# Optimization experiments

Hardware: AMD Instinct MI355X
Metric: run time of the kernel (lower is better)

The kernel has to match this reference:

```python
import jax, jax.numpy as jnp
import numpy as np

B, N, D = 8, 2048, 1024
A_STDP, TAU_STDP, W_OFF, T_MAX = 0.9, 0.5, 0.9, 1.0
V_TH, EPS = 1.0, 1e-5


def setup_inputs() -> dict:
    key = jax.random.key(0)
    ks = jax.random.split(key, 6)
    s = 0.02
    inp = {"x": jax.random.normal(ks[0], (B, N, D), dtype=jnp.float32)}
    for i, nm in enumerate(["q", "k", "v"]):
        inp[f"W{nm}"] = jax.random.normal(ks[1 + i], (D, D), dtype=jnp.float32) * s
        inp[f"g{nm}"] = jnp.ones((D,), jnp.float32)
        inp[f"b{nm}"] = jnp.zeros((D,), jnp.float32)
        inp[f"m{nm}"] = jnp.zeros((D,), jnp.float32)
        inp[f"v{nm}"] = jnp.ones((D,), jnp.float32)
    inp["Wo"] = jax.random.normal(ks[4], (D, D), dtype=jnp.float32) * s
    inp["bo"] = jnp.zeros((D,), jnp.float32)
    return inp


def _proj(x, W, g, b, m, v):
    # Linear (no bias) -> BatchNorm1d (inference, running stats) -> LIF first step
    h = x @ W                                     # [B,N,D]
    h = (h - m) * (g * jax.lax.rsqrt(v + EPS)) + b
    # LIF with mem=None: mem = x, spike = sigmoid(4*(mem - v_th))
    return jax.nn.sigmoid(4.0 * (h - V_TH))


def reference(x, Wq, gq, bq, mq, vq, Wk, gk, bk, mk, vk, Wv, gv, bv, mv, vv, Wo, bo):
    Q = _proj(x, Wq, gq, bq, mq, vq)
    K = _proj(x, Wk, gk, bk, mk, vk)
    V = _proj(x, Wv, gv, bv, mv, vv)
    t_Q = T_MAX * (1.0 - Q.mean(axis=-1, keepdims=True))   # [B,N,1]
    t_K = T_MAX * (1.0 - K.mean(axis=-1, keepdims=True))   # [B,N,1]
    delta_t = t_Q - jnp.swapaxes(t_K, 1, 2)                 # [B,N,N]
    f_stdp = A_STDP * jnp.exp(-jnp.abs(delta_t) / TAU_STDP)
    A = jnp.where(delta_t < 0, f_stdp, -f_stdp) + W_OFF     # [B,N,N]
    return (A @ V) @ Wo + bo                                # [B,N,D]
```

## Files before the change

kernel.cpp:

```cpp
#include <hip/hip_runtime.h>

#define B_ 8
#define N_ 2048
#define D_ 1024
#define M_ (B_*N_)
#define SEGS 64
#define EPB (4096/SEGS)
#define CW 256

typedef __attribute__((ext_vector_type(8))) short short8;
typedef __attribute__((ext_vector_type(4))) float floatx4;

__device__ __forceinline__ ushort f2bf(float f) {
  unsigned u = __builtin_bit_cast(unsigned, f);
  return (ushort)((u + 0x7fffu + ((u >> 16) & 1u)) >> 16);
}
__device__ __forceinline__ float bf2f(ushort u) {
  return __builtin_bit_cast(float, ((unsigned)u) << 16);
}
__device__ __forceinline__ void gload16(const void* g, void* l) {
  __builtin_amdgcn_global_load_lds(
      (const __attribute__((address_space(1))) unsigned*)g,
      (__attribute__((address_space(3))) unsigned*)l, 16, 0, 0);
}
__device__ __forceinline__ float sig4(float h) {
  return 1.0f / (1.0f + __expf(4.0f - 4.0f*h));
}

__global__ __launch_bounds__(256) void conv_x_k(const float4* __restrict__ x,
                                                ushort4* __restrict__ o) {
  int i = blockIdx.x * 256 + threadIdx.x;
  float4 f = x[i];
  ushort4 u;
  u.x = f2bf(f.x); u.y = f2bf(f.y); u.z = f2bf(f.z); u.w = f2bf(f.w);
  o[i] = u;
}

__global__ __launch_bounds__(256) void transpose_k(
    const float* __restrict__ Wq, const float* __restrict__ Wk,
    const float* __restrict__ Wv, const float* __restrict__ Wo,
    ushort* __restrict__ W3T, ushort* __restrict__ WoT) {
  __shared__ float tile[32][33];
  int z = blockIdx.z;
  const float* W = (z == 0) ? Wq : (z == 1) ? Wk : (z == 2) ? Wv : Wo;
  ushort* WT = (z < 3) ? (W3T + (size_t)z * D_ * D_) : WoT;
  int tx = threadIdx.x, ty = threadIdx.y;
  int x = blockIdx.x * 32 + tx;
  int y = blockIdx.y * 32 + ty;
#pragma unroll
  for (int j = 0; j < 32; j += 8)
    tile[ty + j][tx] = W[(size_t)(y + j) * D_ + x];
  __syncthreads();
  int x2 = blockIdx.y * 32 + tx;
  int y2 = blockIdx.x * 32 + ty;
#pragma unroll
  for (int j = 0; j < 32; j += 8)
    WT[(size_t)(y2 + j) * D_ + x2] = f2bf(tile[tx][ty + j]);
}

__device__ __forceinline__ void gemm_mainloop(
    const ushort* __restrict__ Ab, const ushort* __restrict__ Bb,
    ushort* As, ushort* Bs, int t, int wm, int wn, int l15, int quad,
    floatx4 acc[4][4])
{
  int srow[4], soff[4];
#pragma unroll
  for (int r = 0; r < 4; r++) {
    int li = r * 256 + t;
    int row = li >> 3, c = li & 7;
    srow[r] = row;
    soff[r] = ((c - row) & 7) * 8;
  }
  for (int k0 = 0; k0 < D_; k0 += 64) {
    __syncthreads();
#pragma unroll
    for (int r = 0; r < 4; r++) {
      int li = r * 256 + t;
      gload16(Ab + (size_t)srow[r] * D_ + k0 + soff[r], (char*)As + li * 16);
      gload16(Bb + (size_t)srow[r] * D_ + k0 + soff[r], (char*)Bs + li * 16);
    }
    __syncthreads();
#pragma unroll
    for (int s = 0; s < 2; s++) {
      short8 af[4], bfr[4];
#pragma unroll
      for (int tm = 0; tm < 4; tm++) {
        int row = wm * 64 + tm * 16 + l15;
        int p = (s * 4 + quad + row) & 7;
        af[tm] = *(const short8*)(As + row * 64 + p * 8);
      }
#pragma unroll
      for (int tn = 0; tn < 4; tn++) {
        int row = wn * 64 + tn * 16 + l15;
        int p = (s * 4 + quad + row) & 7;
        bfr[tn] = *(const short8*)(Bs + row * 64 + p * 8);
      }
#pragma unroll
      for (int tm = 0; tm < 4; tm++)
#pragma unroll
        for (int tn = 0; tn < 4; tn++)
          acc[tm][tn] = __builtin_amdgcn_mfma_f32_16x16x32_bf16(af[tm], bfr[tn], acc[tm][tn], 0, 0, 0);
    }
  }
}

__global__ __launch_bounds__(256) void gemm_qkv_k(
    const ushort* __restrict__ A, const ushort* __restrict__ W3T,
    const float* __restrict__ gq, const float* __restrict__ bq,
    const float* __restrict__ mq, const float* __restrict__ vq,
    const float* __restrict__ gk, const float* __restrict__ bk,
    const float* __restrict__ mk, const float* __restrict__ vk,
    const float* __restrict__ gv, const float* __restrict__ bv,
    const float* __restrict__ mv, const float* __restrict__ vv,
    float* __restrict__ rsQ, float* __restrict__ rsK, ushort* __restrict__ Vb)
{
  __shared__ ushort As[128 * 64];
  __shared__ ushort Bs[128 * 64];
  const int t = threadIdx.x;
  const int lane = t & 63, wid = t >> 6;
  const int quad = lane >> 4, l15 = lane & 15;
  const int wm = wid >> 1, wn = wid & 1;

  const int lin = blockIdx.x;
  const int xcd = lin & 7, s = lin >> 3;
  const int z   = s >> 7;
  const int yg  = (s >> 6) & 1;
  const int yi  = (s >> 3) & 7;
  const int xzi = s & 7;
  const int tileM = (xcd * 16 + yg * 8 + yi) * 128;
  const int tileN = xzi * 128;

  floatx4 acc[4][4];
#pragma unroll
  for (int i = 0; i < 4; i++)
#pragma unroll
    for (int j = 0; j < 4; j++) acc[i][j] = (floatx4){0.f, 0.f, 0.f, 0.f};

  const ushort* Ab = A + (size_t)tileM * D_;
  const ushort* Bb = W3T + (size_t)z * D_ * D_ + (size_t)tileN * D_;
  gemm_mainloop(Ab, Bb, As, Bs, t, wm, wn, l15, quad, acc);

  const float* gg = (z == 0) ? gq : (z == 1) ? gk : gv;
  const float* bb = (z == 0) ? bq : (z == 1) ? bk : bv;
  const float* mmn = (z == 0) ? mq : (z == 1) ? mk : mv;
  const float* vvn = (z == 0) ? vq : (z == 1) ? vk : vv;

  if (z == 2) {
#pragma unroll
    for (int tn = 0; tn < 4; tn++) {
      int col = tileN + wn * 64 + tn * 16 + l15;
      float sc = gg[col] * rsqrtf(vvn[col] + 1e-5f);
      float sh = bb[col] - mmn[col] * sc;
#pragma unroll
      for (int tm = 0; tm < 4; tm++) {
        int row0 = tileM + wm * 64 + tm * 16 + quad * 4;
#pragma unroll
        for (int r = 0; r < 4; r++)
          Vb[(size_t)(row0 + r) * D_ + col] = f2bf(sig4(acc[tm][tn][r] * sc + sh));
      }
    }
  } else {
    float* rowsum = (z == 0) ? rsQ : rsK;
    float rs[4][4];
#pragma unroll
    for (int tm = 0; tm < 4; tm++)
#pragma unroll
      for (int r = 0; r < 4; r++) rs[tm][r] = 0.f;
#pragma unroll
    for (int tn = 0; tn < 4; tn++) {
      int col = tileN + wn * 64 + tn * 16 + l15;
      float sc = gg[col] * rsqrtf(vvn[col] + 1e-5f);
      float sh = bb[col] - mmn[col] * sc;
#pragma unroll
      for (int tm = 0; tm < 4; tm++)
#pragma unroll
        for (int r = 0; r < 4; r++)
          rs[tm][r] += sig4(acc[tm][tn][r] * sc + sh);
    }
#pragma unroll
    for (int off = 1; off < 16; off <<= 1)
#pragma unroll
      for (int tm = 0; tm < 4; tm++)
#pragma unroll
        for (int r = 0; r < 4; r++)
          rs[tm][r] += __shfl_xor(rs[tm][r], off, 64);
    if (l15 == 0) {
#pragma unroll
      for (int tm = 0; tm < 4; tm++) {
        int row0 = tileM + wm * 64 + tm * 16 + quad * 4;
#pragma unroll
        for (int r = 0; r < 4; r++)
          atomicAdd(&rowsum[row0 + r], rs[tm][r]);
      }
    }
  }
}

__global__ __launch_bounds__(256) void gemm_out_k(
    const ushort* __restrict__ A, const ushort* __restrict__ Bt,
    float* __restrict__ outF, const float* __restrict__ bo)
{
  __shared__ ushort As[128 * 64];
  __shared__ ushort Bs[128 * 64];
  const int t = threadIdx.x;
  const int lane = t & 63, wid = t >> 6;
  const int quad = lane >> 4, l15 = lane & 15;
  const int wm = wid >> 1, wn = wid & 1;

  const int lin = blockIdx.x;
  const int xcd = lin & 7, s = lin >> 3;
  const int yg = s >> 6, yi = (s >> 3) & 7, xi = s & 7;
  const int tileM = (xcd * 16 + yg * 8 + yi) * 128;
  const int tileN = xi * 128;

  floatx4 acc[4][4];
#pragma unroll
  for (int i = 0; i < 4; i++)
#pragma unroll
    for (int j = 0; j < 4; j++) acc[i][j] = (floatx4){0.f, 0.f, 0.f, 0.f};

  const ushort* Ab = A + (size_t)tileM * D_;
  const ushort* Bb = Bt + (size_t)tileN * D_;
  gemm_mainloop(Ab, Bb, As, Bs, t, wm, wn, l15, quad, acc);

#pragma unroll
  for (int tn = 0; tn < 4; tn++) {
    int col = tileN + wn * 64 + tn * 16 + l15;
    float bias = bo[col];
#pragma unroll
    for (int tm = 0; tm < 4; tm++) {
      int row0 = tileM + wm * 64 + tm * 16 + quad * 4;
#pragma unroll
      for (int r = 0; r < 4; r++)
        outF[(size_t)(row0 + r) * D_ + col] = acc[tm][tn][r] + bias;
    }
  }
}

__global__ __launch_bounds__(256) void rank_events_k(
    const float* __restrict__ rsQ, const float* __restrict__ rsK,
    int* __restrict__ evt_tag, float* __restrict__ evt_wa, float* __restrict__ evt_wd)
{
  __shared__ unsigned long long keys[4096];
  __shared__ int part[256];
  int b = blockIdx.y, chunk = blockIdx.x;
  int t = threadIdx.x;
  for (int i = t; i < 4096; i += 256) {
    float v; unsigned tag;
    if (i < 2048) {
      v = 1.0f - rsQ[b * N_ + i] * (1.0f / 1024.0f);
      tag = (unsigned)i | 0x10000u;
    } else {
      int j = i - 2048;
      v = 1.0f - rsK[b * N_ + j] * (1.0f / 1024.0f);
      tag = (unsigned)j;
    }
    keys[i] = ((unsigned long long)__builtin_bit_cast(unsigned, v) << 32) | tag;
  }
  __syncthreads();
  int e = chunk * 128 + (t & 127);
  int j0 = (t >> 7) * 2048;
  unsigned long long me = keys[e];
  int r = 0;
#pragma unroll 8
  for (int j = 0; j < 2048; j++) r += (keys[j0 + j] < me) ? 1 : 0;
  part[t] = r;
  __syncthreads();
  if (t < 128) {
    int rank = part[t] + part[t + 128];
    unsigned tag = (unsigned)(me & 0x1FFFFu);
    float v = __builtin_bit_cast(float, (unsigned)(me >> 32));
    bool isq = (tag & 0x10000u) != 0;
    int o = b * 4096 + rank;
    evt_tag[o] = (int)tag;
    evt_wa[o] = isq ? expf(-2.0f * v) : expf(2.0f * v);
    evt_wd[o] = isq ? expf(2.0f * v) : expf(-2.0f * v);
  }
}

__global__ __launch_bounds__(256) void seg_tot_k(
    const int* __restrict__ evt_tag, const float* __restrict__ evt_wa,
    const float* __restrict__ evt_wd, const ushort* __restrict__ Vb,
    float* __restrict__ totWA, float* __restrict__ totWD, float* __restrict__ totP)
{
  __shared__ int srow[EPB];
  __shared__ float swa[EPB], swd[EPB], spw[EPB];
  int b = blockIdx.z, seg = blockIdx.y, chunk = blockIdx.x;
  int t = threadIdx.x;
  int e0 = b * 4096 + seg * EPB;
  if (t < EPB) {
    int tg = evt_tag[e0 + t];
    bool isk = !(tg & 0x10000);
    srow[t] = isk ? (tg & 0xFFFF) : 0;
    swa[t] = isk ? evt_wa[e0 + t] : 0.f;
    swd[t] = isk ? evt_wd[e0 + t] : 0.f;
    spw[t] = isk ? 1.f : 0.f;
  }
  __syncthreads();
  int c = chunk * 512 + t * 2;
  const ushort* vb = Vb + (size_t)b * N_ * D_ + c;
  float wa0 = 0, wa1 = 0, wd0 = 0, wd1 = 0, p0 = 0, p1 = 0;
#pragma unroll 8
  for (int e = 0; e < EPB; e++) {
    unsigned raw = *(const unsigned*)(vb + (size_t)srow[e] * D_);
    float v0 = bf2f((ushort)(raw & 0xffffu)), v1 = bf2f((ushort)(raw >> 16));
    float wa = swa[e], wd = swd[e], pw = spw[e];
    wa0 += wa * v0; wa1 += wa * v1;
    wd0 += wd * v0; wd1 += wd * v1;
    p0 += pw * v0;  p1 += pw * v1;
  }
  size_t o = ((size_t)b * SEGS + seg) * D_ + c;
  totWA[o] = wa0; totWA[o + 1] = wa1;
  totWD[o] = wd0; totWD[o + 1] = wd1;
  totP[o]  = p0;  totP[o + 1]  = p1;
}

__global__ __launch_bounds__(256) void seg_prefix_k(
    const float* __restrict__ totWA, const float* __restrict__ totWD,
    const float* __restrict__ totP,
    float* __restrict__ preA, float* __restrict__ prePA,
    float* __restrict__ sufD, float* __restrict__ sufPD)
{
  int b = blockIdx.y;
  int c = blockIdx.x * 256 + threadIdx.x;
  float a = 0, pa = 0;
  for (int s = 0; s < SEGS; s++) {
    size_t o = ((size_t)b * SEGS + s) * D_ + c;
    preA[o] = a; prePA[o] = pa;
    a += totWA[o]; pa += totP[o];
  }
  float d = 0, pd = 0;
  for (int s = SEGS - 1; s >= 0; s--) {
    size_t o = ((size_t)b * SEGS + s) * D_ + c;
    sufD[o] = d; sufPD[o] = pd;
    d += totWD[o]; pd += totP[o];
  }
}

__global__ __launch_bounds__(256) void scan_both_k(
    const int* __restrict__ evt_tag, const float* __restrict__ evt_wa,
    const float* __restrict__ evt_wd, const ushort* __restrict__ Vb,
    const float* __restrict__ preA, const float* __restrict__ prePA,
    const float* __restrict__ sufD, const float* __restrict__ sufPD,
    float* AVpart, ushort* __restrict__ AVb)
{
  __shared__ ushort Vt[EPB * CW];
  __shared__ int sisq[EPB], sidx[EPB];
  __shared__ float skwa[EPB], skwd[EPB], sqwa[EPB], sqwd[EPB], spk[EPB];
  int b = blockIdx.z, seg = blockIdx.y, chunk = blockIdx.x;
  int t = threadIdx.x;
  int e0 = b * 4096 + seg * EPB;
  if (t < EPB) {
    int tg = evt_tag[e0 + t];
    bool isq = (tg & 0x10000) != 0;
    float wa = evt_wa[e0 + t], wd = evt_wd[e0 + t];
    sisq[t] = isq; sidx[t] = isq ? (tg & 0xFFFF) : 0;
    skwa[t] = isq ? 0.f : wa;  sqwa[t] = wa;
    skwd[t] = isq ? 0.f : wd;  sqwd[t] = wd;
    spk[t]  = isq ? 0.f : 1.f;
  }
  __syncthreads();
  int c0 = chunk * CW;
  const ushort* vbase = Vb + (size_t)b * N_ * D_ + c0;
  __shared__ int srow[EPB];
  if (t < EPB) {
    int tg = evt_tag[e0 + t];
    srow[t] = (tg & 0x10000) ? 0 : (tg & 0xFFFF);
  }
  __syncthreads();
#pragma unroll
  for (int r = 0; r < 8; r++) {
    int li = r * 256 + t;
    int e = li >> 5, ch = li & 31;
    gload16(vbase + (size_t)srow[e] * D_ + ch * 8, (char*)Vt + li * 16);
  }
  __syncthreads();

  int cth = c0 + t;
  size_t po = ((size_t)b * SEGS + seg) * D_ + cth;
  float* AVrow = AVpart + (size_t)b * N_ * D_ + cth;
  ushort* AVbrow = AVb + (size_t)b * N_ * D_ + cth;

  {
    float s = preA[po], p = prePA[po];
#pragma unroll 4
    for (int e = 0; e < EPB; e++) {
      float v = bf2f(Vt[e * CW + t]);
      if (sisq[e]) AVrow[(size_t)sidx[e] * D_] = 0.9f * (p - sqwa[e] * s);
      s += skwa[e] * v; p += spk[e] * v;
    }
  }
  {
    float s = sufD[po], p = sufPD[po];
#pragma unroll 4
    for (int e = EPB - 1; e >= 0; e--) {
      float v = bf2f(Vt[e * CW + t]);
      if (sisq[e]) {
        size_t o = (size_t)sidx[e] * D_;
        AVbrow[o] = f2bf(AVrow[o] + 0.9f * (p + sqwd[e] * s));
      }
      s += skwd[e] * v; p += spk[e] * v;
    }
  }
}

extern "C" void kernel_launch(void* const* d_in, const int* in_sizes, int n_in,
                              void* d_out, int out_size, void* d_ws, size_t ws_size,
                              hipStream_t stream) {
  (void)in_sizes; (void)n_in; (void)out_size; (void)ws_size;
  const float* x  = (const float*)d_in[0];
  const float* Wq = (const float*)d_in[1];
  const float* gq = (const float*)d_in[2];
  const float* bq = (const float*)d_in[3];
  const float* mq = (const float*)d_in[4];
  const float* vq = (const float*)d_in[5];
  const float* Wk = (const float*)d_in[6];
  const float* gk = (const float*)d_in[7];
  const float* bk = (const float*)d_in[8];
  const float* mk = (const float*)d_in[9];
  const float* vk = (const float*)d_in[10];
  const float* Wv = (const float*)d_in[11];
  const float* gv = (const float*)d_in[12];
  const float* bv = (const float*)d_in[13];
  const float* mv = (const float*)d_in[14];
  const float* vv = (const float*)d_in[15];
  const float* Wo = (const float*)d_in[16];
  const float* bo = (const float*)d_in[17];

  char* p = (char*)d_ws;
  auto alloc = [&](size_t n) { char* r = p; p += n; return r; };
  ushort* x16  = (ushort*)alloc((size_t)M_ * D_ * 2);
  ushort* Vb   = (ushort*)alloc((size_t)M_ * D_ * 2);
  ushort* AVb  = (ushort*)alloc((size_t)M_ * D_ * 2);
  ushort* W3T  = (ushort*)alloc((size_t)3 * D_ * D_ * 2);
  ushort* WoT  = (ushort*)alloc((size_t)D_ * D_ * 2);
  float*  rsQ  = (float*)alloc((size_t)M_ * 4);
  float*  rsK  = (float*)alloc((size_t)M_ * 4);
  int*    evt_tag = (int*)alloc((size_t)B_ * 4096 * 4);
  float*  evt_wa  = (float*)alloc((size_t)B_ * 4096 * 4);
  float*  evt_wd  = (float*)alloc((size_t)B_ * 4096 * 4);
  float*  totWA   = (float*)alloc((size_t)B_ * SEGS * D_ * 4);
  float*  totWD   = (float*)alloc((size_t)B_ * SEGS * D_ * 4);
  float*  totP    = (float*)alloc((size_t)B_ * SEGS * D_ * 4);
  float*  preA    = (float*)alloc((size_t)B_ * SEGS * D_ * 4);
  float*  prePA   = (float*)alloc((size_t)B_ * SEGS * D_ * 4);
  float*  sufD    = (float*)alloc((size_t)B_ * SEGS * D_ * 4);
  float*  sufPD   = (float*)alloc((size_t)B_ * SEGS * D_ * 4);

  hipMemsetAsync(rsQ, 0, (size_t)2 * M_ * 4, stream);

  conv_x_k<<<(M_ * D_) / 1024, 256, 0, stream>>>((const float4*)x, (ushort4*)x16);
  dim3 tb(32, 8), tg(32, 32, 4);
  transpose_k<<<tg, tb, 0, stream>>>(Wq, Wk, Wv, Wo, W3T, WoT);

  gemm_qkv_k<<<3072, 256, 0, stream>>>(x16, W3T, gq, bq, mq, vq,
                                       gk, bk, mk, vk, gv, bv, mv, vv,
                                       rsQ, rsK, Vb);

  rank_events_k<<<dim3(32, B_), 256, 0, stream>>>(rsQ, rsK, evt_tag, evt_wa, evt_wd);

  seg_tot_k<<<dim3(2, SEGS, B_), 256, 0, stream>>>(evt_tag, evt_wa, evt_wd, Vb,
                                                   totWA, totWD, totP);
  seg_prefix_k<<<dim3(D_ / 256, B_), 256, 0, stream>>>(totWA, totWD, totP,
                                                       preA, prePA, sufD, sufPD);
  scan_both_k<<<dim3(D_ / CW, SEGS, B_), 256, 0, stream>>>(
      evt_tag, evt_wa, evt_wd, Vb, preA, prePA, sufD, sufPD, (float*)d_out, AVb);

  gemm_out_k<<<1024, 256, 0, stream>>>(AVb, WoT, (float*)d_out, bo);
}
```

Measured before the change: 471.7 us.

## Rewrite GEMM mainloops as 256x256 tiles with 4-stage async LDS pipeline

Both bf16 GEMMs (QKV projection and output projection) now use 256x256 block tiles with 512 threads and a K-step of 32. Four LDS stages are filled by global_load_lds prefetch three steps ahead, with explicit vmcnt waits and split barriers so loads overlap MFMA work. s_setprio is raised around the MFMA bursts. BN scale/shift and bias are hoisted before the loop. The larger tiles cut global traffic per FLOP, but they raise register and LDS pressure (128KB LDS per block) and leave fewer blocks to fill the GPU.

```diff
diff --git a/kernel.cpp b/kernel.cpp
--- a/kernel.cpp
+++ b/kernel.cpp
@@ -58,53 +58,99 @@
     WT[(size_t)(y2 + j) * D_ + x2] = f2bf(tile[tx][ty + j]);
 }
 
-__device__ __forceinline__ void gemm_mainloop(
+__device__ __forceinline__ void mainloop256(
     const ushort* __restrict__ Ab, const ushort* __restrict__ Bb,
-    ushort* As, ushort* Bs, int t, int wm, int wn, int l15, int quad,
-    floatx4 acc[4][4])
-{
-  int srow[4], soff[4];
-#pragma unroll
-  for (int r = 0; r < 4; r++) {
-    int li = r * 256 + t;
-    int row = li >> 3, c = li & 7;
-    srow[r] = row;
-    soff[r] = ((c - row) & 7) * 8;
-  }
-  for (int k0 = 0; k0 < D_; k0 += 64) {
-    __syncthreads();
-#pragma unroll
-    for (int r = 0; r < 4; r++) {
-      int li = r * 256 + t;
-      gload16(Ab + (size_t)srow[r] * D_ + k0 + soff[r], (char*)As + li * 16);
-      gload16(Bb + (size_t)srow[r] * D_ + k0 + soff[r], (char*)Bs + li * 16);
-    }
-    __syncthreads();
-#pragma unroll
-    for (int s = 0; s < 2; s++) {
-      short8 af[4], bfr[4];
-#pragma unroll
-      for (int tm = 0; tm < 4; tm++) {
-        int row = wm * 64 + tm * 16 + l15;
-        int p = (s * 4 + quad + row) & 7;
-        af[tm] = *(const short8*)(As + row * 64 + p * 8);
-      }
-#pragma unroll
-      for (int tn = 0; tn < 4; tn++) {
-        int row = wn * 64 + tn * 16 + l15;
-        int p = (s * 4 + quad + row) & 7;
-        bfr[tn] = *(const short8*)(Bs + row * 64 + p * 8);
-      }
-#pragma unroll
-      for (int tm = 0; tm < 4; tm++)
-#pragma unroll
-        for (int tn = 0; tn < 4; tn++)
-          acc[tm][tn] = __builtin_amdgcn_mfma_f32_16x16x32_bf16(af[tm], bfr[tn], acc[tm][tn], 0, 0, 0);
-    }
-  }
-}
-
-__global__ __launch_bounds__(256) void gemm_qkv_k(
+    ushort* __restrict__ As, ushort* __restrict__ Bs, int t,
+    floatx4 (&acc)[8][4])
+{
+  const int lane = t & 63, wid = t >> 6;
+  const int quad = lane >> 4, l15 = lane & 15;
+  const int wm = wid >> 2, wn = wid & 3;
+
+  int srcO[2], dsto[2];
+#pragma unroll
+  for (int r = 0; r < 2; r++) {
+    int li = r * 512 + t;
+    int row = li >> 2, c = li & 3;
+    int soff = ((c - (row >> 1)) & 3) * 8;
+    srcO[r] = row * D_ + soff;
+    dsto[r] = li * 16;
+  }
+
+  int offA[8], offB[4];
+#pragma unroll
+  for (int i = 0; i < 8; i++) {
+    int row = wm * 128 + i * 16 + l15;
+    offA[i] = row * 32 + ((quad + (row >> 1)) & 3) * 8;
+  }
+#pragma unroll
+  for (int i = 0; i < 4; i++) {
+    int row = wn * 64 + i * 16 + l15;
+    offB[i] = row * 32 + ((quad + (row >> 1)) & 3) * 8;
+  }
+
+#pragma unroll
+  for (int pt = 0; pt < 3; pt++) {
+#pragma unroll
+    for (int r = 0; r < 2; r++)
+      gload16(Ab + srcO[r] + pt * 32, (char*)(As + pt * 8192) + dsto[r]);
+#pragma unroll
+    for (int r = 0; r < 2; r++)
+      gload16(Bb + srcO[r] + pt * 32, (char*)(Bs + pt * 8192) + dsto[r]);
+  }
+
+  const int NT = D_ / 32;
+#pragma unroll 4
+  for (int tt = 0; tt < NT; tt++) {
+    if (tt < NT - 2)       asm volatile("s_waitcnt vmcnt(8)" ::: "memory");
+    else if (tt == NT - 2) asm volatile("s_waitcnt vmcnt(4)" ::: "memory");
+    else                   asm volatile("s_waitcnt vmcnt(0)" ::: "memory");
+    __builtin_amdgcn_s_barrier();
+    const ushort* Asl = As + (tt & 3) * 8192;
+    const ushort* Bsl = Bs + (tt & 3) * 8192;
+    const bool pf = (tt + 3 < NT);
+
+    if (pf) {
+      ushort* d = As + ((tt + 3) & 3) * 8192;
+#pragma unroll
+      for (int r = 0; r < 2; r++)
+        gload16(Ab + srcO[r] + (tt + 3) * 32, (char*)d + dsto[r]);
+    }
+    short8 af[4], bf[4];
+#pragma unroll
+    for (int i = 0; i < 4; i++) af[i] = *(const short8*)(Asl + offA[i]);
+#pragma unroll
+    for (int i = 0; i < 4; i++) bf[i] = *(const short8*)(Bsl + offB[i]);
+    __builtin_amdgcn_s_setprio(1);
+#pragma unroll
+    for (int tm = 0; tm < 4; tm++)
+#pragma unroll
+      for (int tn = 0; tn < 4; tn++)
+        acc[tm][tn] = __builtin_amdgcn_mfma_f32_16x16x32_bf16(
+            af[tm], bf[tn], acc[tm][tn], 0, 0, 0);
+    __builtin_amdgcn_s_setprio(0);
+    __builtin_amdgcn_s_barrier();
+
+    if (pf) {
+      ushort* d = Bs + ((tt + 3) & 3) * 8192;
+#pragma unroll
+      for (int r = 0; r < 2; r++)
+        gload16(Bb + srcO[r] + (tt + 3) * 32, (char*)d + dsto[r]);
+    }
+#pragma unroll
+    for (int i = 0; i < 4; i++) af[i] = *(const short8*)(Asl + offA[4 + i]);
+    __builtin_amdgcn_s_setprio(1);
+#pragma unroll
+    for (int tm = 0; tm < 4; tm++)
+#pragma unroll
+      for (int tn = 0; tn < 4; tn++)
+        acc[4 + tm][tn] = __builtin_amdgcn_mfma_f32_16x16x32_bf16(
+            af[tm], bf[tn], acc[4 + tm][tn], 0, 0, 0);
+    __builtin_amdgcn_s_setprio(0);
+  }
+}
+
+__global__ __launch_bounds__(512, 2) void gemm_qkv_k(
     const ushort* __restrict__ A, const ushort* __restrict__ W3T,
     const float* __restrict__ gq, const float* __restrict__ bq,
     const float* __restrict__ mq, const float* __restrict__ vq,
@@ -114,125 +160,125 @@
     const float* __restrict__ mv, const float* __restrict__ vv,
     float* __restrict__ rsQ, float* __restrict__ rsK, ushort* __restrict__ Vb)
 {
-  __shared__ ushort As[128 * 64];
-  __shared__ ushort Bs[128 * 64];
+  __shared__ ushort As[4 * 8192];
+  __shared__ ushort Bs[4 * 8192];
   const int t = threadIdx.x;
   const int lane = t & 63, wid = t >> 6;
   const int quad = lane >> 4, l15 = lane & 15;
-  const int wm = wid >> 1, wn = wid & 1;
+  const int wm = wid >> 2, wn = wid & 3;
 
   const int lin = blockIdx.x;
   const int xcd = lin & 7, s = lin >> 3;
-  const int z   = s >> 7;
-  const int yg  = (s >> 6) & 1;
-  const int yi  = (s >> 3) & 7;
-  const int xzi = s & 7;
-  const int tileM = (xcd * 16 + yg * 8 + yi) * 128;
-  const int tileN = xzi * 128;
-
-  floatx4 acc[4][4];
-#pragma unroll
-  for (int i = 0; i < 4; i++)
-#pragma unroll
-    for (int j = 0; j < 4; j++) acc[i][j] = (floatx4){0.f, 0.f, 0.f, 0.f};
-
-  const ushort* Ab = A + (size_t)tileM * D_;
-  const ushort* Bb = W3T + (size_t)z * D_ * D_ + (size_t)tileN * D_;
-  gemm_mainloop(Ab, Bb, As, Bs, t, wm, wn, l15, quad, acc);
-
-  const float* gg = (z == 0) ? gq : (z == 1) ? gk : gv;
-  const float* bb = (z == 0) ? bq : (z == 1) ? bk : bv;
+  const int z = s >> 5;
+  const int rem = s & 31;
+  const int mg = rem >> 2;
+  const int nt = rem & 3;
+  const int tileM = (xcd * 8 + mg) * 256;
+  const int tileN = nt * 256;
+
+  const float* gg  = (z == 0) ? gq : (z == 1) ? gk : gv;
+  const float* bb  = (z == 0) ? bq : (z == 1) ? bk : bv;
   const float* mmn = (z == 0) ? mq : (z == 1) ? mk : mv;
   const float* vvn = (z == 0) ? vq : (z == 1) ? vk : vv;
 
+  float sc[4], sh[4];
+#pragma unroll
+  for (int tn = 0; tn < 4; tn++) {
+    int col = tileN + wn * 64 + tn * 16 + l15;
+    float scv = gg[col] * rsqrtf(vvn[col] + 1e-5f);
+    sc[tn] = scv;
+    sh[tn] = bb[col] - mmn[col] * scv;
+  }
+  asm volatile("s_waitcnt vmcnt(0)" ::: "memory");
+
+  floatx4 acc[8][4];
+#pragma unroll
+  for (int i = 0; i < 8; i++)
+#pragma unroll
+    for (int j = 0; j < 4; j++) acc[i][j] = (floatx4){0.f, 0.f, 0.f, 0.f};
+
+  mainloop256(A + (size_t)tileM * D_,
+              W3T + (size_t)z * D_ * D_ + (size_t)tileN * D_,
+              As, Bs, t, acc);
+
   if (z == 2) {
 #pragma unroll
-    for (int tn = 0; tn < 4; tn++) {
-      int col = tileN + wn * 64 + tn * 16 + l15;
-      float sc = gg[col] * rsqrtf(vvn[col] + 1e-5f);
-      float sh = bb[col] - mmn[col] * sc;
-#pragma unroll
-      for (int tm = 0; tm < 4; tm++) {
-        int row0 = tileM + wm * 64 + tm * 16 + quad * 4;
+    for (int tm = 0; tm < 8; tm++) {
+      int row0 = tileM + wm * 128 + tm * 16 + quad * 4;
+#pragma unroll
+      for (int tn = 0; tn < 4; tn++) {
+        int col = tileN + wn * 64 + tn * 16 + l15;
 #pragma unroll
         for (int r = 0; r < 4; r++)
-          Vb[(size_t)(row0 + r) * D_ + col] = f2bf(sig4(acc[tm][tn][r] * sc + sh));
+          Vb[(size_t)(row0 + r) * D_ + col] =
+              f2bf(sig4(acc[tm][tn][r] * sc[tn] + sh[tn]));
       }
     }
   } else {
     float* rowsum = (z == 0) ? rsQ : rsK;
-    float rs[4][4];
-#pragma unroll
-    for (int tm = 0; tm < 4; tm++)
-#pragma unroll
-      for (int r = 0; r < 4; r++) rs[tm][r] = 0.f;
-#pragma unroll
-    for (int tn = 0; tn < 4; tn++) {
-      int col = tileN + wn * 64 + tn * 16 + l15;
-      float sc = gg[col] * rsqrtf(vvn[col] + 1e-5f);
-      float sh = bb[col] - mmn[col] * sc;
-#pragma unroll
-      for (int tm = 0; tm < 4; tm++)
+#pragma unroll
+    for (int tm = 0; tm < 8; tm++) {
+      float rs[4] = {0.f, 0.f, 0.f, 0.f};
+#pragma unroll
+      for (int tn = 0; tn < 4; tn++)
 #pragma unroll
         for (int r = 0; r < 4; r++)
-          rs[tm][r] += sig4(acc[tm][tn][r] * sc + sh);
-    }
-#pragma unroll
-    for (int off = 1; off < 16; off <<= 1)
-#pragma unroll
-      for (int tm = 0; tm < 4; tm++)
+          rs[r] += sig4(acc[tm][tn][r] * sc[tn] + sh[tn]);
+#pragma unroll
+      for (int off = 1; off < 16; off <<= 1)
 #pragma unroll
         for (int r = 0; r < 4; r++)
-          rs[tm][r] += __shfl_xor(rs[tm][r], off, 64);
-    if (l15 == 0) {
-#pragma unroll
-      for (int tm = 0; tm < 4; tm++) {
-        int row0 = tileM + wm * 64 + tm * 16 + quad * 4;
+          rs[r] += __shfl_xor(rs[r], off, 64);
+      if (l15 == 0) {
+        int row0 = tileM + wm * 128 + tm * 16 + quad * 4;
 #pragma unroll
         for (int r = 0; r < 4; r++)
-          atomicAdd(&rowsum[row0 + r], rs[tm][r]);
+          atomicAdd(&rowsum[row0 + r], rs[r]);
       }
     }
   }
 }
 
-__global__ __launch_bounds__(256) void gemm_out_k(
+__global__ __launch_bounds__(512, 2) void gemm_out_k(
     const ushort* __restrict__ A, const ushort* __restrict__ Bt,
     float* __restrict__ outF, const float* __restrict__ bo)
 {
-  __shared__ ushort As[128 * 64];
-  __shared__ ushort Bs[128 * 64];
+  __shared__ ushort As[4 * 8192];
+  __shared__ ushort Bs[4 * 8192];
   const int t = threadIdx.x;
   const int lane = t & 63, wid = t >> 6;
   const int quad = lane >> 4, l15 = lane & 15;
-  const int wm = wid >> 1, wn = wid & 1;
+  const int wm = wid >> 2, wn = wid & 3;
 
   const int lin = blockIdx.x;
   const int xcd = lin & 7, s = lin >> 3;
-  const int yg = s >> 6, yi = (s >> 3) & 7, xi = s & 7;
-  const int tileM = (xcd * 16 + yg * 8 + yi) * 128;
-  const int tileN = xi * 128;
-
-  floatx4 acc[4][4];
-#pragma unroll
-  for (int i = 0; i < 4; i++)
+  const int mg = s >> 2, nt = s & 3;
+  const int tileM = (xcd * 8 + mg) * 256;
+  const int tileN = nt * 256;
+
+  float bias[4];
+#pragma unroll
+  for (int tn = 0; tn < 4; tn++)
+    bias[tn] = bo[tileN + wn * 64 + tn * 16 + l15];
+  asm volatile("s_waitcnt vmcnt(0)" ::: "memory");
+
+  floatx4 acc[8][4];
+#pragma unroll
+  for (int i = 0; i < 8; i++)
 #pragma unroll
     for (int j = 0; j < 4; j++) acc[i][j] = (floatx4){0.f, 0.f, 0.f, 0.f};
 
-  const ushort* Ab = A + (size_t)tileM * D_;
-  const ushort* Bb = Bt + (size_t)tileN * D_;
-  gemm_mainloop(Ab, Bb, As, Bs, t, wm, wn, l15, quad, acc);
-
-#pragma unroll
-  for (int tn = 0; tn < 4; tn++) {
-    int col = tileN + wn * 64 + tn * 16 + l15;
-    float bias = bo[col];
-#pragma unroll
-    for (int tm = 0; tm < 4; tm++) {
-      int row0 = tileM + wm * 64 + tm * 16 + quad * 4;
+  mainloop256(A + (size_t)tileM * D_, Bt + (size_t)tileN * D_, As, Bs, t, acc);
+
+#pragma unroll
+  for (int tm = 0; tm < 8; tm++) {
+    int row0 = tileM + wm * 128 + tm * 16 + quad * 4;
+#pragma unroll
+    for (int tn = 0; tn < 4; tn++) {
+      int col = tileN + wn * 64 + tn * 16 + l15;
 #pragma unroll
       for (int r = 0; r < 4; r++)
-        outF[(size_t)(row0 + r) * D_ + col] = acc[tm][tn][r] + bias;
+        outF[(size_t)(row0 + r) * D_ + col] = acc[tm][tn][r] + bias[tn];
     }
   }
 }
@@ -453,9 +499,9 @@
   dim3 tb(32, 8), tg(32, 32, 4);
   transpose_k<<<tg, tb, 0, stream>>>(Wq, Wk, Wv, Wo, W3T, WoT);
 
-  gemm_qkv_k<<<3072, 256, 0, stream>>>(x16, W3T, gq, bq, mq, vq,
-                                       gk, bk, mk, vk, gv, bv, mv, vv,
-                                       rsQ, rsK, Vb);
+  gemm_qkv_k<<<768, 512, 0, stream>>>(x16, W3T, gq, bq, mq, vq,
+                                      gk, bk, mk, vk, gv, bv, mv, vv,
+                                      rsQ, rsK, Vb);
 
   rank_events_k<<<dim3(32, B_), 256, 0, stream>>>(rsQ, rsK, evt_tag, evt_wa, evt_wd);
 
@@ -466,5 +512,5 @@
   scan_both_k<<<dim3(D_ / CW, SEGS, B_), 256, 0, stream>>>(
       evt_tag, evt_wa, evt_wd, Vb, preA, prePA, sufD, sufPD, (float*)d_out, AVb);
 
-  gemm_out_k<<<1024, 256, 0, stream>>>(AVb, WoT, (float*)d_out, bo);
-}
+  gemm_out_k<<<256, 512, 0, stream>>>(AVb, WoT, (float*)d_out, bo);
+}
```

Result: faster. 443.3 us (-6.0%).
